# Kernel optimization log

Measured on AMD Instinct MI355X. Metric: run time of the kernel, lower is better.

The kernel has to match this reference:

```python
import jax, jax.numpy as jnp
import numpy as np

B, C, H, W = 32, 512, 64, 64
K = 512  # num_embeddings == embedding_dim == C (required by the original view())
COMMIT = 0.25


def setup_inputs() -> dict:
    key = jax.random.key(0)
    k1, k2 = jax.random.split(key)
    x = jax.random.normal(k1, (B, C, H, W), dtype=jnp.float32)
    # nn.Embedding weight init: uniform(-1/K, 1/K)
    embed = jax.random.uniform(k2, (K, C), dtype=jnp.float32, minval=-1.0 / K, maxval=1.0 / K)
    return {"x": x, "embed": embed}


def reference(x, embed):
    # BCHW -> BHWC
    inputs = jnp.transpose(x, (0, 2, 3, 1))  # [B,H,W,C]
    flat = inputs.reshape(-1, C)              # [N,C], N = B*H*W
    d = (jnp.sum(flat * flat, axis=1, keepdims=True)
         + jnp.sum(embed * embed, axis=1)
         - 2.0 * flat @ embed.T)              # [N,K]
    idx = jnp.argmin(d, axis=1)               # [N]
    # one-hot @ embed  ==  gather
    quantized = embed[idx].reshape(inputs.shape)  # [B,H,W,C]

    e_latent = jnp.mean((jax.lax.stop_gradient(quantized) - inputs) ** 2)
    q_latent = jnp.mean((quantized - jax.lax.stop_gradient(inputs)) ** 2)
    loss = q_latent + COMMIT * e_latent

    # straight-through estimator
    quant_st = inputs + jax.lax.stop_gradient(quantized - inputs)

    # perplexity (as in source: mean over batch of #unique codes used)
    idx_b = idx.reshape(B, -1)                # [B, H*W]

    def n_unique(i):
        cnt = jnp.zeros((K,), jnp.int32).at[i].add(1)
        return jnp.sum(cnt > 0)

    perplexity = jnp.mean(jax.vmap(n_unique)(idx_b).astype(jnp.float32))

    return loss, jnp.transpose(quant_st, (0, 3, 1, 2)), perplexity, idx_b
```

## Files before the change

kernel.cpp:

```cpp
#include <hip/hip_runtime.h>
#include <stdint.h>

#define B_ 32
#define C_ 512
#define HW_ 4096
#define N_ 131072
#define K_ 512
#define QELEMS 67108864
#define MARGIN 1e-3f
#define CAND   2.5e-3f
#define MAXC   16
#define RFCAP 131072

typedef __attribute__((ext_vector_type(8)))  short bf16x8;
typedef __attribute__((ext_vector_type(16))) float f32x16;

__device__ __forceinline__ ushort f2bf(float f) {
  uint u = __float_as_uint(f);
  return (ushort)((u + 0x7FFFu + ((u >> 16) & 1u)) >> 16);
}

__device__ __forceinline__ float np_pw512(const float* a) {
  float P[4];
#pragma unroll
  for (int m = 0; m < 4; ++m) {
    const float* q = a + m * 128;
    float rv[16];
#pragma unroll
    for (int l = 0; l < 16; ++l) {
      float v0 = q[l],      v1 = q[16 + l],  v2 = q[32 + l],  v3 = q[48 + l];
      float v4 = q[64 + l], v5 = q[80 + l],  v6 = q[96 + l],  v7 = q[112 + l];
      rv[l] = ((v0 + v1) + (v2 + v3)) + ((v4 + v5) + (v6 + v7));
    }
    float u[8], w[4];
#pragma unroll
    for (int l = 0; l < 8; ++l) u[l] = rv[8 + l] + rv[l];
#pragma unroll
    for (int l = 0; l < 4; ++l) w[l] = u[4 + l] + u[l];
    P[m] = (w[0] + w[2]) + (w[1] + w[3]);
  }
  return (P[0] + P[1]) + (P[2] + P[3]);
}

__device__ __forceinline__ float np_pw512_sq(const float* a) {
  float P[4];
#pragma unroll
  for (int m = 0; m < 4; ++m) {
    const float* q = a + m * 128;
    float rv[16];
#pragma unroll
    for (int l = 0; l < 16; ++l) {
      float v0 = __fmul_rn(q[l], q[l]);
      float v1 = __fmul_rn(q[16 + l], q[16 + l]);
      float v2 = __fmul_rn(q[32 + l], q[32 + l]);
      float v3 = __fmul_rn(q[48 + l], q[48 + l]);
      float v4 = __fmul_rn(q[64 + l], q[64 + l]);
      float v5 = __fmul_rn(q[80 + l], q[80 + l]);
      float v6 = __fmul_rn(q[96 + l], q[96 + l]);
      float v7 = __fmul_rn(q[112 + l], q[112 + l]);
      rv[l] = ((v0 + v1) + (v2 + v3)) + ((v4 + v5) + (v6 + v7));
    }
    float u[8], w[4];
#pragma unroll
    for (int l = 0; l < 8; ++l) u[l] = rv[8 + l] + rv[l];
#pragma unroll
    for (int l = 0; l < 4; ++l) w[l] = u[4 + l] + u[l];
    P[m] = (w[0] + w[2]) + (w[1] + w[3]);
  }
  return (P[0] + P[1]) + (P[2] + P[3]);
}

__global__ __launch_bounds__(256) void k_prep(const float* __restrict__ embed,
    float* __restrict__ senp, float* __restrict__ eT, int* __restrict__ rcnt,
    int* __restrict__ ocnt, int* __restrict__ candCnt)
{
  __shared__ float sqa[C_];
  int k = blockIdx.x;
  candCnt[blockIdx.x * 256 + threadIdx.x] = 0;
  for (int c = threadIdx.x; c < C_; c += 256) {
    float e = embed[k * C_ + c];
    eT[c * K_ + k] = e;
    sqa[c] = __fmul_rn(e, e);
  }
  __syncthreads();
  if (threadIdx.x == 0) {
    senp[k] = np_pw512(sqa);
    if (blockIdx.x == 0) { *rcnt = 0; *ocnt = 0; }
  }
}

__global__ __launch_bounds__(256) void k_epack(const float* __restrict__ embed,
    ushort* __restrict__ efrag)
{
  const int cb = blockIdx.x;
  const int t = threadIdx.x;
  const int lane = t & 63, ksq = t >> 6;
  const int l31 = lane & 31, lhi = lane >> 5;
  const float* ep = embed + ((size_t)(cb * 32 + l31) << 9) + lhi * 8;
#pragma unroll
  for (int i = 0; i < 8; ++i) {
    int ks = ksq * 8 + i;
    float4 v0 = *(const float4*)(ep + ks * 16);
    float4 v1 = *(const float4*)(ep + ks * 16 + 4);
    uint u0 = (uint)f2bf(v0.x) | ((uint)f2bf(v0.y) << 16);
    uint u1 = (uint)f2bf(v0.z) | ((uint)f2bf(v0.w) << 16);
    uint u2 = (uint)f2bf(v1.x) | ((uint)f2bf(v1.y) << 16);
    uint u3 = (uint)f2bf(v1.z) | ((uint)f2bf(v1.w) << 16);
    ushort* op = efrag + (((size_t)(cb * 32 + ks)) * 64 + lane) * 8;
    *(uint4*)op = make_uint4(u0, u1, u2, u3);
  }
}

__global__ __launch_bounds__(256) void k_xsplit(const float* __restrict__ x,
    ushort* __restrict__ xfrag, float* __restrict__ xT)
{
  __shared__ float tile[64][66];
  const int bid = blockIdx.x;
  const int ht = bid & 63, ct = (bid >> 6) & 7, b = bid >> 9;
  const int t = threadIdx.x;
  const int r = t & 63, cq = t >> 6;
  const float* xp = x + (((size_t)(b * C_ + ct * 64)) << 12) + ht * 64 + r;
#pragma unroll
  for (int i = 0; i < 16; ++i) {
    int c = cq * 16 + i;
    tile[r][c] = xp[(size_t)c << 12];
  }
  __syncthreads();
  const int lane = t & 63, ksl = t >> 6;
  const int l31 = lane & 31, lhi = lane >> 5;
  const int ks = ct * 4 + ksl;
  const int cc = ksl * 16 + lhi * 8;
#pragma unroll
  for (int rbl = 0; rbl < 2; ++rbl) {
    int rr = rbl * 32 + l31;
    uint u[4];
#pragma unroll
    for (int j = 0; j < 4; ++j) {
      float f0 = tile[rr][cc + 2 * j];
      float f1 = tile[rr][cc + 2 * j + 1];
      u[j] = (uint)f2bf(f0) | ((uint)f2bf(f1) << 16);
    }
    size_t rb = (size_t)b * 128 + ht * 2 + rbl;
    ushort* op = xfrag + ((rb * 32 + ks) * 64 + lane) * 8;
    *(uint4*)op = make_uint4(u[0], u[1], u[2], u[3]);
  }
  if (xT) {
    const int r2 = t >> 2, cs2 = (t & 3) << 4;
    float* op = xT + ((size_t)(b * HW_ + ht * 64 + r2) << 9) + ct * 64 + cs2;
#pragma unroll
    for (int j = 0; j < 4; ++j) {
      float4 v;
      v.x = tile[r2][cs2 + 4 * j + 0];
      v.y = tile[r2][cs2 + 4 * j + 1];
      v.z = tile[r2][cs2 + 4 * j + 2];
      v.w = tile[r2][cs2 + 4 * j + 3];
      *(float4*)(op + 4 * j) = v;
    }
  }
}

__global__ __launch_bounds__(512, 2) void k_argmin(const ushort* __restrict__ xfrag,
    const ushort* __restrict__ efrag, const float* __restrict__ senp,
    int* __restrict__ idx_out, int* __restrict__ rcnt, int* __restrict__ rrows,
    int* __restrict__ candCnt, int* __restrict__ cand)
{
  __shared__ float ses[K_];
  __shared__ float mbL[128][4], msL[128][4];
  __shared__ int   miL[128][4];
  __shared__ float rowBest[128];
  __shared__ int   rowFlag[128];
  __shared__ __align__(16) ushort stg[2 * 20 * 512];
  const int t = threadIdx.x;
  const int lane = t & 63, wid = t >> 6;
  const int wc = wid & 3, wr = wid >> 2;
  const int l31 = lane & 31, lhi = lane >> 5;
  const int bid = blockIdx.x;

  for (int i = t; i < K_; i += 512) ses[i] = senp[i];

  const ushort* g0 = (wid < 4)
      ? xfrag + ((size_t)(bid * 4 + wid) * 2048 + lane) * 8
      : efrag + ((size_t)(wid - 4) * 2048 + lane) * 8;
  const ushort* g1 = efrag + ((size_t)(wid + 4) * 2048 + lane) * 8;
  const ushort* g2 = efrag + ((size_t)(wid + 12) * 2048 + lane) * 8;

  auto GLL = [&](const ushort* gp, int lofs) {
    __builtin_amdgcn_global_load_lds(
        (const __attribute__((address_space(1))) uint32_t*)gp,
        (__attribute__((address_space(3))) uint32_t*)&stg[lofs], 16, 0, 0);
  };

  GLL(g0, wid * 512);
  GLL(g1, (wid + 8) * 512);
  if (wid < 4) GLL(g2, (wid + 16) * 512);
  __syncthreads();

  f32x16 z = {0,0,0,0,0,0,0,0,0,0,0,0,0,0,0,0};
  f32x16 a00 = z, a01 = z, a02 = z, a03 = z;
  f32x16 a10 = z, a11 = z, a12 = z, a13 = z;

  for (int ks = 0; ks < 32; ++ks) {
    const int cur = ks & 1;
    if (ks + 1 < 32) {
      const size_t so = (size_t)(ks + 1) * 512;
      const int bo = (cur ^ 1) * (20 * 512);
      GLL(g0 + so, bo + wid * 512);
      GLL(g1 + so, bo + (wid + 8) * 512);
      if (wid < 4) GLL(g2 + so, bo + (wid + 16) * 512);
    }
    const ushort* bp = &stg[cur * (20 * 512)];
    bf16x8 x0 = *(const bf16x8*)(bp + (wr * 2 + 0) * 512 + lane * 8);
    bf16x8 x1 = *(const bf16x8*)(bp + (wr * 2 + 1) * 512 + lane * 8);
    bf16x8 e0 = *(const bf16x8*)(bp + (4 + wc * 4 + 0) * 512 + lane * 8);
    bf16x8 e1 = *(const bf16x8*)(bp + (4 + wc * 4 + 1) * 512 + lane * 8);
    bf16x8 e2 = *(const bf16x8*)(bp + (4 + wc * 4 + 2) * 512 + lane * 8);
    bf16x8 e3 = *(const bf16x8*)(bp + (4 + wc * 4 + 3) * 512 + lane * 8);
    __builtin_amdgcn_s_setprio(1);
    a00 = __builtin_amdgcn_mfma_f32_32x32x16_bf16(e0, x0, a00, 0, 0, 0);
    a01 = __builtin_amdgcn_mfma_f32_32x32x16_bf16(e1, x0, a01, 0, 0, 0);
    a02 = __builtin_amdgcn_mfma_f32_32x32x16_bf16(e2, x0, a02, 0, 0, 0);
    a03 = __builtin_amdgcn_mfma_f32_32x32x16_bf16(e3, x0, a03, 0, 0, 0);
    a10 = __builtin_amdgcn_mfma_f32_32x32x16_bf16(e0, x1, a10, 0, 0, 0);
    a11 = __builtin_amdgcn_mfma_f32_32x32x16_bf16(e1, x1, a11, 0, 0, 0);
    a12 = __builtin_amdgcn_mfma_f32_32x32x16_bf16(e2, x1, a12, 0, 0, 0);
    a13 = __builtin_amdgcn_mfma_f32_32x32x16_bf16(e3, x1, a13, 0, 0, 0);
    __builtin_amdgcn_s_setprio(0);
    __syncthreads();
  }

  float b0 = 1e30f, s0 = 1e30f; int i0 = 0;
#pragma unroll
  for (int r = 0; r < 16; ++r) {
    int crow = (r & 3) + 8 * (r >> 2) + 4 * lhi;
    float v; int code;
    code = wc * 128 + 0  + crow; v = ses[code] - 2.0f * a00[r];
    if (v < b0 || (v == b0 && code < i0)) { s0 = b0; b0 = v; i0 = code; }
    else if (v < s0) s0 = v;
    code = wc * 128 + 32 + crow; v = ses[code] - 2.0f * a01[r];
    if (v < b0 || (v == b0 && code < i0)) { s0 = b0; b0 = v; i0 = code; }
    else if (v < s0) s0 = v;
    code = wc * 128 + 64 + crow; v = ses[code] - 2.0f * a02[r];
    if (v < b0 || (v == b0 && code < i0)) { s0 = b0; b0 = v; i0 = code; }
    else if (v < s0) s0 = v;
    code = wc * 128 + 96 + crow; v = ses[code] - 2.0f * a03[r];
    if (v < b0 || (v == b0 && code < i0)) { s0 = b0; b0 = v; i0 = code; }
    else if (v < s0) s0 = v;
  }
  float b1 = 1e30f, s1 = 1e30f; int i1 = 0;
#pragma unroll
  for (int r = 0; r < 16; ++r) {
    int crow = (r & 3) + 8 * (r >> 2) + 4 * lhi;
    float v; int code;
    code = wc * 128 + 0  + crow; v = ses[code] - 2.0f * a10[r];
    if (v < b1 || (v == b1 && code < i1)) { s1 = b1; b1 = v; i1 = code; }
    else if (v < s1) s1 = v;
    code = wc * 128 + 32 + crow; v = ses[code] - 2.0f * a11[r];
    if (v < b1 || (v == b1 && code < i1)) { s1 = b1; b1 = v; i1 = code; }
    else if (v < s1) s1 = v;
    code = wc * 128 + 64 + crow; v = ses[code] - 2.0f * a12[r];
    if (v < b1 || (v == b1 && code < i1)) { s1 = b1; b1 = v; i1 = code; }
    else if (v < s1) s1 = v;
    code = wc * 128 + 96 + crow; v = ses[code] - 2.0f * a13[r];
    if (v < b1 || (v == b1 && code < i1)) { s1 = b1; b1 = v; i1 = code; }
    else if (v < s1) s1 = v;
  }
  const float pb0 = b0, ps0 = s0; const int pi0 = i0;
  const float pb1 = b1, ps1 = s1; const int pi1 = i1;
  {
    float ob = __shfl_xor(b0, 32, 64), os = __shfl_xor(s0, 32, 64);
    int   oi = __shfl_xor(i0, 32, 64);
    float ns = fminf(fmaxf(b0, ob), fminf(s0, os));
    if (ob < b0 || (ob == b0 && oi < i0)) { b0 = ob; i0 = oi; }
    s0 = ns;
  }
  {
    float ob = __shfl_xor(b1, 32, 64), os = __shfl_xor(s1, 32, 64);
    int   oi = __shfl_xor(i1, 32, 64);
    float ns = fminf(fmaxf(b1, ob), fminf(s1, os));
    if (ob < b1 || (ob == b1 && oi < i1)) { b1 = ob; i1 = oi; }
    s1 = ns;
  }
  if (lane < 32) {
    int rr0 = (wr * 2 + 0) * 32 + l31;
    int rr1 = (wr * 2 + 1) * 32 + l31;
    mbL[rr0][wc] = b0; msL[rr0][wc] = s0; miL[rr0][wc] = i0;
    mbL[rr1][wc] = b1; msL[rr1][wc] = s1; miL[rr1][wc] = i1;
  }
  __syncthreads();
  if (t < 128) {
    float Bv = 1e30f, Sv = 1e30f; int Iv = 0;
#pragma unroll
    for (int q = 0; q < 4; ++q) {
      float bq = mbL[t][q], sq = msL[t][q]; int iq = miL[t][q];
      if (bq < Bv || (bq == Bv && iq < Iv)) { Sv = fminf(Bv, sq); Bv = bq; Iv = iq; }
      else Sv = fminf(Sv, bq);
    }
    int n = bid * 128 + t;
    idx_out[n] = Iv;
    rowBest[t] = Bv;
    int fl = (Sv - Bv < MARGIN) ? 1 : 0;
    rowFlag[t] = fl;
    if (fl) {
      int p = atomicAdd(rcnt, 1);
      if (p < RFCAP) rrows[p] = n;
    }
  }
  __syncthreads();
  {
    const int rr0 = (wr * 2 + 0) * 32 + l31;
    if (rowFlag[rr0]) {
      const float thr = rowBest[rr0] + CAND;
      const int n = bid * 128 + rr0;
      if (pb0 <= thr) {
        int p = atomicAdd(&candCnt[n], 1);
        if (p < MAXC) cand[(size_t)n * MAXC + p] = pi0;
      }
      if (ps0 <= thr) {
#pragma unroll
        for (int r = 0; r < 16; ++r) {
          int crow = (r & 3) + 8 * (r >> 2) + 4 * lhi;
          float v; int code;
          code = wc * 128 + 0  + crow; v = ses[code] - 2.0f * a00[r];
          if (v <= thr && code != pi0) { int p = atomicAdd(&candCnt[n], 1); if (p < MAXC) cand[(size_t)n * MAXC + p] = code; }
          code = wc * 128 + 32 + crow; v = ses[code] - 2.0f * a01[r];
          if (v <= thr && code != pi0) { int p = atomicAdd(&candCnt[n], 1); if (p < MAXC) cand[(size_t)n * MAXC + p] = code; }
          code = wc * 128 + 64 + crow; v = ses[code] - 2.0f * a02[r];
          if (v <= thr && code != pi0) { int p = atomicAdd(&candCnt[n], 1); if (p < MAXC) cand[(size_t)n * MAXC + p] = code; }
          code = wc * 128 + 96 + crow; v = ses[code] - 2.0f * a03[r];
          if (v <= thr && code != pi0) { int p = atomicAdd(&candCnt[n], 1); if (p < MAXC) cand[(size_t)n * MAXC + p] = code; }
        }
      }
    }
    const int rr1 = (wr * 2 + 1) * 32 + l31;
    if (rowFlag[rr1]) {
      const float thr = rowBest[rr1] + CAND;
      const int n = bid * 128 + rr1;
      if (pb1 <= thr) {
        int p = atomicAdd(&candCnt[n], 1);
        if (p < MAXC) cand[(size_t)n * MAXC + p] = pi1;
      }
      if (ps1 <= thr) {
#pragma unroll
        for (int r = 0; r < 16; ++r) {
          int crow = (r & 3) + 8 * (r >> 2) + 4 * lhi;
          float v; int code;
          code = wc * 128 + 0  + crow; v = ses[code] - 2.0f * a10[r];
          if (v <= thr && code != pi1) { int p = atomicAdd(&candCnt[n], 1); if (p < MAXC) cand[(size_t)n * MAXC + p] = code; }
          code = wc * 128 + 32 + crow; v = ses[code] - 2.0f * a11[r];
          if (v <= thr && code != pi1) { int p = atomicAdd(&candCnt[n], 1); if (p < MAXC) cand[(size_t)n * MAXC + p] = code; }
          code = wc * 128 + 64 + crow; v = ses[code] - 2.0f * a12[r];
          if (v <= thr && code != pi1) { int p = atomicAdd(&candCnt[n], 1); if (p < MAXC) cand[(size_t)n * MAXC + p] = code; }
          code = wc * 128 + 96 + crow; v = ses[code] - 2.0f * a13[r];
          if (v <= thr && code != pi1) { int p = atomicAdd(&candCnt[n], 1); if (p < MAXC) cand[(size_t)n * MAXC + p] = code; }
        }
      }
    }
  }
}

__global__ __launch_bounds__(256) void k_refine(const float* __restrict__ x,
    const float* __restrict__ xT, const float* __restrict__ embed,
    const float* __restrict__ senp,
    const int* __restrict__ rcnt, const int* __restrict__ rrows,
    const int* __restrict__ candCnt, const int* __restrict__ cand,
    int* __restrict__ ocnt, int* __restrict__ olist,
    int* __restrict__ idx_out)
{
  __shared__ float xls[4][516];
  __shared__ float SxSh[4];
  __shared__ int   nrow[4];
  const int t = threadIdx.x;
  const int lane = t & 63, w = t >> 6;
  int cnt = *rcnt; if (cnt > RFCAP) cnt = RFCAP;
  for (int base = blockIdx.x * 4; base < cnt; base += gridDim.x * 4) {
    __syncthreads();
    if (t < 4) {
      int i = base + t;
      nrow[t] = rrows[i < cnt ? i : base];
    }
    __syncthreads();
    if (xT) {
      for (int i = t; i < 4 * C_; i += 256) {
        int s = i >> 9, c = i & 511;
        xls[s][c] = xT[((size_t)nrow[s] << 9) + c];
      }
    } else {
      for (int i = t; i < 4 * C_; i += 256) {
        int s = i >> 9, c = i & 511;
        int n = nrow[s];
        int b = n >> 12, hw = n & 4095;
        xls[s][c] = x[(((size_t)(b * C_ + c)) << 12) + hw];
      }
    }
    __syncthreads();
    if (t < 4) SxSh[t] = np_pw512_sq(&xls[t][0]);
    __syncthreads();
    const int n = nrow[w];
    const int cc = candCnt[n];
    float d = 1e30f; int code = 0x7fffffff;
    if (cc <= MAXC) {
      if (lane < cc) {
        code = cand[(size_t)n * MAXC + lane];
        const float* e = embed + (size_t)code * C_;
        const float* xr = &xls[w][0];
        float s1 = 0.f, s2 = 0.f;
        for (int c = 0; c < 384; ++c)  s1 = fmaf(xr[c], e[c], s1);
        for (int c = 384; c < 512; ++c) s2 = fmaf(xr[c], e[c], s2);
        float M = s1 + s2;
        d = (SxSh[w] + senp[code]) - 2.0f * M;
      }
#pragma unroll
      for (int off = 1; off < 16; off <<= 1) {
        float ov = __shfl_xor(d, off, 64);
        int   oc = __shfl_xor(code, off, 64);
        if (ov < d || (ov == d && oc < code)) { d = ov; code = oc; }
      }
      if (lane == 0 && base + w < cnt) idx_out[n] = code;
    } else {
      if (lane == 0 && base + w < cnt) {
        int p = atomicAdd(ocnt, 1);
        if (p < RFCAP) olist[p] = n;
      }
    }
  }
}

__global__ __launch_bounds__(512) void k_refine_full(const float* __restrict__ x,
    const float* __restrict__ xT, const float* __restrict__ eT,
    const float* __restrict__ senp,
    const int* __restrict__ rcnt, const int* __restrict__ rrows,
    int* __restrict__ idx_out)
{
  __shared__ float xls[8][520];
  __shared__ float SxSh[8];
  __shared__ int   nrow[8];
  __shared__ float wval[8][8];
  __shared__ int   widx[8][8];
  const int t = threadIdx.x;
  const int lane = t & 63, w = t >> 6;
  int cnt = *rcnt; if (cnt > RFCAP) cnt = RFCAP;
  for (int base = blockIdx.x * 8; base < cnt; base += gridDim.x * 8) {
    __syncthreads();
    if (t < 8) {
      int i = base + t;
      nrow[t] = rrows[i < cnt ? i : base];
    }
    __syncthreads();
    if (xT) {
#pragma unroll
      for (int rr = 0; rr < 8; ++rr)
        xls[rr][t] = xT[((size_t)nrow[rr] << 9) + t];
    } else {
#pragma unroll
      for (int rr = 0; rr < 8; ++rr) {
        int n = nrow[rr];
        int b = n >> 12, hw = n & 4095;
        xls[rr][t] = x[(((size_t)(b * C_ + t)) << 12) + hw];
      }
    }
    __syncthreads();
    if (t < 8) SxSh[t] = np_pw512_sq(&xls[t][0]);
    __syncthreads();
    const float* ep = eT + t;
    float a1[8], a2[8];
#pragma unroll
    for (int rr = 0; rr < 8; ++rr) { a1[rr] = 0.f; a2[rr] = 0.f; }
    for (int c4 = 0; c4 < 384; c4 += 4) {
      float e0 = ep[(size_t)(c4 + 0) << 9];
      float e1 = ep[(size_t)(c4 + 1) << 9];
      float e2 = ep[(size_t)(c4 + 2) << 9];
      float e3 = ep[(size_t)(c4 + 3) << 9];
#pragma unroll
      for (int rr = 0; rr < 8; ++rr) {
        float4 xv = *(const float4*)&xls[rr][c4];
        a1[rr] = fmaf(xv.x, e0, a1[rr]);
        a1[rr] = fmaf(xv.y, e1, a1[rr]);
        a1[rr] = fmaf(xv.z, e2, a1[rr]);
        a1[rr] = fmaf(xv.w, e3, a1[rr]);
      }
    }
    for (int c4 = 384; c4 < 512; c4 += 4) {
      float e0 = ep[(size_t)(c4 + 0) << 9];
      float e1 = ep[(size_t)(c4 + 1) << 9];
      float e2 = ep[(size_t)(c4 + 2) << 9];
      float e3 = ep[(size_t)(c4 + 3) << 9];
#pragma unroll
      for (int rr = 0; rr < 8; ++rr) {
        float4 xv = *(const float4*)&xls[rr][c4];
        a2[rr] = fmaf(xv.x, e0, a2[rr]);
        a2[rr] = fmaf(xv.y, e1, a2[rr]);
        a2[rr] = fmaf(xv.z, e2, a2[rr]);
        a2[rr] = fmaf(xv.w, e3, a2[rr]);
      }
    }
    float se = senp[t];
    float bv[8]; int bi[8];
#pragma unroll
    for (int rr = 0; rr < 8; ++rr) {
      float M = a1[rr] + a2[rr];
      bv[rr] = (SxSh[rr] + se) - 2.0f * M;
      bi[rr] = t;
    }
#pragma unroll
    for (int off = 1; off < 64; off <<= 1) {
#pragma unroll
      for (int rr = 0; rr < 8; ++rr) {
        float ov = __shfl_xor(bv[rr], off, 64);
        int   oi = __shfl_xor(bi[rr], off, 64);
        if (ov < bv[rr] || (ov == bv[rr] && oi < bi[rr])) { bv[rr] = ov; bi[rr] = oi; }
      }
    }
    if (lane == 0) {
#pragma unroll
      for (int rr = 0; rr < 8; ++rr) { wval[w][rr] = bv[rr]; widx[w][rr] = bi[rr]; }
    }
    __syncthreads();
    if (t < 8) {
      float Bv = wval[0][t]; int Iv = widx[0][t];
#pragma unroll
      for (int q = 1; q < 8; ++q) {
        float ov = wval[q][t]; int oi = widx[q][t];
        if (ov < Bv || (ov == Bv && oi < Iv)) { Bv = ov; Iv = oi; }
      }
      if (base + t < cnt) idx_out[nrow[t]] = Iv;
    }
  }
}

__global__ __launch_bounds__(256) void k_gather(const float* __restrict__ x,
    const float* __restrict__ embed, const int* __restrict__ idx,
    float* __restrict__ out_q, double* __restrict__ loss_part)
{
  __shared__ float ecol[32][512];
  const int bid = blockIdx.x;
  const int hch = bid & 1, cch = (bid >> 1) & 15, b = bid >> 5;
  const int c0 = cch * 32, hw0 = hch * 2048;
  const int t = threadIdx.x;
  for (int i = t; i < 512 * 32; i += 256) {
    int c = i & 31, k = i >> 5;
    ecol[c][(k + c0 + c) & 511] = embed[((size_t)k << 9) + c0 + c];
  }
  __syncthreads();
  int kreg[8];
#pragma unroll
  for (int j = 0; j < 8; ++j)
    kreg[j] = idx[(b << 12) + hw0 + t + 256 * j];
  double s = 0.0;
  for (int c = 0; c < 32; ++c) {
    const float* xrow = x + (((size_t)(b * C_ + c0 + c)) << 12) + hw0;
    float* orow = out_q + (((size_t)(b * C_ + c0 + c)) << 12) + hw0;
#pragma unroll
    for (int j = 0; j < 8; ++j) {
      float q  = ecol[c][(kreg[j] + c0 + c) & 511];
      float xv = xrow[t + 256 * j];
      orow[t + 256 * j] = q;
      double d = (double)q - (double)xv;
      s += d * d;
    }
  }
  for (int off = 32; off > 0; off >>= 1) s += __shfl_down(s, off, 64);
  __shared__ double wsum[4];
  if ((t & 63) == 0) wsum[t >> 6] = s;
  __syncthreads();
  if (t == 0)
    loss_part[bid] = (wsum[0] + wsum[1]) + (wsum[2] + wsum[3]);
}

__global__ __launch_bounds__(256) void k_pplx(const int* __restrict__ idx,
    float* __restrict__ out_idxf, int* __restrict__ counts)
{
  __shared__ int flags[K_];
  __shared__ int red[256];
  int b = blockIdx.x;
  for (int i = threadIdx.x; i < K_; i += 256) flags[i] = 0;
  __syncthreads();
  for (int hw = threadIdx.x; hw < HW_; hw += 256) {
    int k = idx[(b << 12) + hw];
    flags[k] = 1;
    out_idxf[(b << 12) + hw] = (float)k;
  }
  __syncthreads();
  int c = 0;
  for (int i = threadIdx.x; i < K_; i += 256) c += flags[i];
  red[threadIdx.x] = c;
  __syncthreads();
  for (int st = 128; st > 0; st >>= 1) {
    if (threadIdx.x < st) red[threadIdx.x] += red[threadIdx.x + st];
    __syncthreads();
  }
  if (threadIdx.x == 0) counts[b] = red[0];
}

__global__ __launch_bounds__(256) void k_final(const double* __restrict__ loss_part,
    const int* __restrict__ counts, float* __restrict__ out_loss,
    float* __restrict__ out_pplx)
{
  __shared__ double sred[256];
  double s = 0.0;
  for (int i = threadIdx.x; i < 1024; i += 256) s += loss_part[i];
  sred[threadIdx.x] = s;
  __syncthreads();
  for (int st = 128; st > 0; st >>= 1) {
    if (threadIdx.x < st) sred[threadIdx.x] += sred[threadIdx.x + st];
    __syncthreads();
  }
  if (threadIdx.x == 0) {
    *out_loss = (float)(1.25 * sred[0] / (double)QELEMS);
    int c = 0;
    for (int i = 0; i < B_; ++i) c += counts[i];
    *out_pplx = (float)c / (float)B_;
  }
}

extern "C" void kernel_launch(void* const* d_in, const int* in_sizes, int n_in,
                              void* d_out, int out_size, void* d_ws, size_t ws_size,
                              hipStream_t stream)
{
  const float* x     = (const float*)d_in[0];
  const float* embed = (const float*)d_in[1];
  float* out      = (float*)d_out;
  float* out_loss = out;
  float* out_q    = out + 1;
  float* out_pplx = out + 1 + QELEMS;
  float* out_idxf = out + 2 + QELEMS;

  char* ws = (char*)d_ws;
  int*    w_idx = (int*)ws;
  double* w_lp  = (double*)(ws + 524288);
  int*    w_cnt = (int*)(ws + 524288 + 16384);
  size_t pers = 524288 + 16384 + 128;

  const size_t SZ_XFR  = 134217728;
  const size_t SZ_EFR  = 524288;
  const size_t SZ_SENP = 2048;
  const size_t SZ_RCNT = 256;
  const size_t SZ_RROW = (size_t)RFCAP * 4;
  const size_t SZ_OLST = (size_t)RFCAP * 4;
  const size_t SZ_ET   = (size_t)K_ * C_ * 4;
  const size_t SZ_CCNT = (size_t)N_ * 4;
  const size_t SZ_CAND = (size_t)N_ * MAXC * 4;
  const size_t SZ_XT   = (size_t)N_ * C_ * 4;
  const size_t VOL_SMALL = SZ_XFR + SZ_EFR + SZ_SENP + SZ_RCNT + SZ_RROW +
                           SZ_OLST + SZ_ET + SZ_CCNT + SZ_CAND;
  const size_t VOL_BIG   = VOL_SMALL + SZ_XT;

  char* vbase;
  float* w_xT = nullptr;
  if (ws_size >= pers + VOL_BIG + 4096) {
    vbase = ws + ((pers + 255) & ~(size_t)255);
    w_xT  = (float*)(vbase + VOL_SMALL);
  } else if (ws_size >= pers + VOL_SMALL + 4096) {
    vbase = ws + ((pers + 255) & ~(size_t)255);
  } else {
    uintptr_t a = ((uintptr_t)(out_q + QELEMS) - VOL_SMALL) & ~(uintptr_t)255;
    vbase = (char*)a;
  }
  char* p = vbase;
  ushort* w_xfr  = (ushort*)p;            p += SZ_XFR;
  ushort* w_efr  = (ushort*)p;            p += SZ_EFR;
  float*  w_senp = (float*)p;             p += SZ_SENP;
  int*    w_rcnt = (int*)p;
  int*    w_ocnt = (int*)(p + 128);       p += SZ_RCNT;
  int*    w_rrows= (int*)p;               p += SZ_RROW;
  int*    w_olst = (int*)p;               p += SZ_OLST;
  float*  w_eT   = (float*)p;             p += SZ_ET;
  int*    w_ccnt = (int*)p;               p += SZ_CCNT;
  int*    w_cand = (int*)p;               p += SZ_CAND;

  k_prep  <<<dim3(512),   dim3(256), 0, stream>>>(embed, w_senp, w_eT, w_rcnt, w_ocnt, w_ccnt);
  k_epack <<<dim3(16),    dim3(256), 0, stream>>>(embed, w_efr);
  k_xsplit<<<dim3(16384), dim3(256), 0, stream>>>(x, w_xfr, w_xT);
  k_argmin<<<dim3(1024),  dim3(512), 0, stream>>>(w_xfr, w_efr, w_senp, w_idx, w_rcnt, w_rrows, w_ccnt, w_cand);
  k_refine<<<dim3(2048),  dim3(256), 0, stream>>>(x, w_xT, embed, w_senp, w_rcnt, w_rrows, w_ccnt, w_cand, w_ocnt, w_olst, w_idx);
  k_refine_full<<<dim3(256), dim3(512), 0, stream>>>(x, w_xT, w_eT, w_senp, w_ocnt, w_olst, w_idx);
  k_gather<<<dim3(1024),  dim3(256), 0, stream>>>(x, embed, w_idx, out_q, w_lp);
  k_pplx  <<<dim3(32),    dim3(256), 0, stream>>>(w_idx, out_idxf, w_cnt);
  k_final <<<dim3(1),     dim3(256), 0, stream>>>(w_lp, w_cnt, out_loss, out_pplx);
}
```

Baseline: 523.9 us.

## Triple-buffer LDS staging with partial vmcnt waits in argmin GEMM loop

Moves the argmin kernel's global-to-LDS staging from double to triple buffering, prefetching two k-steps ahead. Each wave waits with a partial vmcnt instead of a full __syncthreads drain, so loads stay in flight across iterations. The cost is extra LDS (about 20KB more), which may threaten occupancy at 2 blocks/CU, and a hand-counted vmcnt that depends on exact load counts per wave.

Result: slower. 545.2 us (+4.1%).

```diff
diff --git a/kernel.cpp b/kernel.cpp
--- a/kernel.cpp
+++ b/kernel.cpp
@@ -169,14 +169,17 @@
   __shared__ int   miL[128][4];
   __shared__ float rowBest[128];
   __shared__ int   rowFlag[128];
-  __shared__ __align__(16) ushort stg[2 * 20 * 512];
+  __shared__ __align__(16) ushort stg[3 * 20 * 512];
   const int t = threadIdx.x;
   const int lane = t & 63, wid = t >> 6;
   const int wc = wid & 3, wr = wid >> 2;
   const int l31 = lane & 31, lhi = lane >> 5;
   const int bid = blockIdx.x;
+  const int CH = 20 * 512;
 
   for (int i = t; i < K_; i += 512) ses[i] = senp[i];
+  asm volatile("s_waitcnt vmcnt(0) lgkmcnt(0)" ::: "memory");
+  __builtin_amdgcn_s_barrier();
 
   const ushort* g0 = (wid < 4)
       ? xfrag + ((size_t)(bid * 4 + wid) * 2048 + lane) * 8
@@ -190,25 +193,35 @@
         (__attribute__((address_space(3))) uint32_t*)&stg[lofs], 16, 0, 0);
   };
 
-  GLL(g0, wid * 512);
-  GLL(g1, (wid + 8) * 512);
-  if (wid < 4) GLL(g2, (wid + 16) * 512);
-  __syncthreads();
+  GLL(g0, 0 * CH + wid * 512);
+  GLL(g1, 0 * CH + (wid + 8) * 512);
+  if (wid < 4) GLL(g2, 0 * CH + (wid + 16) * 512);
+  GLL(g0 + 512, 1 * CH + wid * 512);
+  GLL(g1 + 512, 1 * CH + (wid + 8) * 512);
+  if (wid < 4) GLL(g2 + 512, 1 * CH + (wid + 16) * 512);
 
   f32x16 z = {0,0,0,0,0,0,0,0,0,0,0,0,0,0,0,0};
   f32x16 a00 = z, a01 = z, a02 = z, a03 = z;
   f32x16 a10 = z, a11 = z, a12 = z, a13 = z;
 
   for (int ks = 0; ks < 32; ++ks) {
-    const int cur = ks & 1;
-    if (ks + 1 < 32) {
-      const size_t so = (size_t)(ks + 1) * 512;
-      const int bo = (cur ^ 1) * (20 * 512);
-      GLL(g0 + so, bo + wid * 512);
-      GLL(g1 + so, bo + (wid + 8) * 512);
-      if (wid < 4) GLL(g2 + so, bo + (wid + 16) * 512);
-    }
-    const ushort* bp = &stg[cur * (20 * 512)];
+    const int slot = ks % 3;
+    if (ks + 2 < 32) {
+      const int wslot = (ks + 2) % 3;
+      const size_t so = (size_t)(ks + 2) * 512;
+      GLL(g0 + so, wslot * CH + wid * 512);
+      GLL(g1 + so, wslot * CH + (wid + 8) * 512);
+      if (wid < 4) GLL(g2 + so, wslot * CH + (wid + 16) * 512);
+    }
+    if (ks < 30) {
+      if (wid < 4) asm volatile("s_waitcnt vmcnt(6)" ::: "memory");
+      else         asm volatile("s_waitcnt vmcnt(4)" ::: "memory");
+    } else {
+      asm volatile("s_waitcnt vmcnt(0)" ::: "memory");
+    }
+    __builtin_amdgcn_sched_barrier(0);
+    __builtin_amdgcn_s_barrier();
+    const ushort* bp = &stg[slot * CH];
     bf16x8 x0 = *(const bf16x8*)(bp + (wr * 2 + 0) * 512 + lane * 8);
     bf16x8 x1 = *(const bf16x8*)(bp + (wr * 2 + 1) * 512 + lane * 8);
     bf16x8 e0 = *(const bf16x8*)(bp + (4 + wc * 4 + 0) * 512 + lane * 8);
@@ -225,7 +238,8 @@
     a12 = __builtin_amdgcn_mfma_f32_32x32x16_bf16(e2, x1, a12, 0, 0, 0);
     a13 = __builtin_amdgcn_mfma_f32_32x32x16_bf16(e3, x1, a13, 0, 0, 0);
     __builtin_amdgcn_s_setprio(0);
-    __syncthreads();
+    __builtin_amdgcn_sched_barrier(0);
+    __builtin_amdgcn_s_barrier();
   }
 
   float b0 = 1e30f, s0 = 1e30f; int i0 = 0;
```
